# Optimization experiments

Measured on AMD Instinct MI355X. Metric: run time of the kernel, lower is better.

The kernel has to match this reference:

```python
import jax, jax.numpy as jnp
import numpy as np

B, T, D = 8, 512, 1024
H, DQK, DV = 16, 128, 128  # n_heads, d_qk = emb_dim//h_qk, d_v = emb_dim//h_v


def setup_inputs() -> dict:
    key = jax.random.key(0)
    ks = jax.random.split(key, 8)
    s = 0.02
    return {
        "X": jax.random.normal(ks[0], (B, T, D), jnp.float32),
        "pos_enc_k": jax.random.normal(ks[1], (T, T, DQK), jnp.float32) * s,
        "pos_enc_v": jax.random.normal(ks[2], (T, T, DV), jnp.float32) * s,
        "Wq": jax.random.normal(ks[3], (D, H * DQK), jnp.float32) * s,
        "bq": jnp.zeros((H * DQK,), jnp.float32),
        "Wk": jax.random.normal(ks[4], (D, H * DQK), jnp.float32) * s,
        "bk": jnp.zeros((H * DQK,), jnp.float32),
        "Wv": jax.random.normal(ks[5], (D, H * DV), jnp.float32) * s,
        "bv": jnp.zeros((H * DV,), jnp.float32),
        "Wp": jax.random.normal(ks[6], (H * DV, D), jnp.float32) * s,
        "bp": jnp.zeros((D,), jnp.float32),
    }


def reference(X, pos_enc_k, pos_enc_v, Wq, bq, Wk, bk, Wv, bv, Wp, bp):
    b, t, d = X.shape
    # projections -> (b, h, t, dhead)
    Q = (X @ Wq + bq).reshape(b, t, H, DQK).transpose(0, 2, 1, 3)
    K = (X @ Wk + bk).reshape(b, t, H, DQK).transpose(0, 2, 1, 3)
    V = (X @ Wv + bv).reshape(b, t, H, DV).transpose(0, 2, 1, 3)
    # content attention + relative-position key bias
    att = jnp.einsum("bhqd,bhkd->bhqk", Q, K)
    att = att + jnp.einsum("bhqd,qkd->bhqk", Q, pos_enc_k)
    att = att / jnp.sqrt(jnp.asarray(DQK, X.dtype))
    # causal mask (do_mask=True)
    causal = jnp.tril(jnp.ones((t, t), bool))
    att = jnp.where(causal[None, None], att, jnp.asarray(-jnp.inf, att.dtype))
    att = jax.nn.softmax(att, axis=-1)
    # values + relative-position value correction
    y = jnp.einsum("bhqk,bhkd->bhqd", att, V)
    y = y + jnp.einsum("bhqk,qkd->bhqd", att, pos_enc_v)
    y = y.transpose(0, 2, 1, 3).reshape(b, t, H * DV)
    return y @ Wp + bp
```

## Files before the change

### kernel.cpp

```cpp
#include <hip/hip_runtime.h>
#include <stdint.h>

#define B_  8
#define T_  512
#define D_  1024
#define H_  16
#define DH  128
#define BH  128
#define ND  2048
#define BT  4096

typedef __attribute__((ext_vector_type(8))) short          short8;
typedef __attribute__((ext_vector_type(8))) __bf16         bf16x8;
typedef __attribute__((ext_vector_type(4))) float          f32x4;
typedef __attribute__((ext_vector_type(4))) unsigned short ushort4v;

static __device__ __forceinline__ unsigned short f2bf(float f) {
  unsigned u = __builtin_bit_cast(unsigned, f);
  u += 0x7FFFu + ((u >> 16) & 1u);
  return (unsigned short)(u >> 16);
}
static __device__ __forceinline__ float bf2f(unsigned short h) {
  unsigned u = ((unsigned)h) << 16;
  return __builtin_bit_cast(float, u);
}
static __device__ __forceinline__ f32x4 mfma16(short8 a, short8 b, f32x4 c) {
  return __builtin_amdgcn_mfma_f32_16x16x32_bf16(
      __builtin_bit_cast(bf16x8, a), __builtin_bit_cast(bf16x8, b), c, 0, 0, 0);
}
static __device__ __forceinline__ void gload16(const unsigned short* g, unsigned short* l) {
  __builtin_amdgcn_global_load_lds(
      (const __attribute__((address_space(1))) void*)g,
      (__attribute__((address_space(3))) void*)l, 16, 0, 0);
}

template <int ROWS>
static __device__ __forceinline__ void stage_sw64(unsigned short* lds,
                                                  const unsigned short* __restrict__ src,
                                                  long stride, int tid) {
#pragma unroll
  for (int it = 0; it < ROWS / 32; ++it) {
    int n = tid + it * 256;
    int r = n >> 3, c = (n & 7) ^ (r & 7);
    gload16(src + (long)r * stride + c * 8, lds + n * 8);
  }
}

template <int MR, int NR>
static __device__ __forceinline__ void mfma_sw64(const unsigned short* As,
                                                 const unsigned short* Bs,
                                                 int a0, int b0, int lrow, int g,
                                                 f32x4 (*acc)[NR]) {
#pragma unroll
  for (int ks = 0; ks < 2; ++ks) {
    short8 a[MR], b[NR];
#pragma unroll
    for (int i = 0; i < MR; ++i) {
      int ra = a0 + i * 16 + lrow;
      int c = (ks * 4 + g) ^ (ra & 7);
      a[i] = *(const short8*)&As[ra * 64 + c * 8];
    }
#pragma unroll
    for (int j = 0; j < NR; ++j) {
      int rb = b0 + j * 16 + lrow;
      int c = (ks * 4 + g) ^ (rb & 7);
      b[j] = *(const short8*)&Bs[rb * 64 + c * 8];
    }
#pragma unroll
    for (int i = 0; i < MR; ++i)
#pragma unroll
      for (int j = 0; j < NR; ++j) acc[i][j] = mfma16(a[i], b[j], acc[i][j]);
  }
}

#define IDS4                             \
  const int tid  = threadIdx.x;          \
  const int lane = tid & 63;             \
  const int wid  = tid >> 6;             \
  const int lrow = lane & 15;            \
  const int lk8  = (lane >> 4) * 8;      \
  const int lr4  = (lane >> 4) * 4;      \
  const int lg   = lane >> 4;            \
  const int wm = wid >> 1, wn = wid & 1;

#define LTS 132
#define LTQ 68

__global__ __launch_bounds__(256) void k_prep(const float* __restrict__ X,
                                              unsigned short* __restrict__ Xb,
                                              const float* __restrict__ Wq,
                                              const float* __restrict__ Wk,
                                              const float* __restrict__ Wv,
                                              const float* __restrict__ Wp,
                                              unsigned short* __restrict__ WT,
                                              unsigned short* __restrict__ WpT) {
  __shared__ float tile[32][33];
  int bid = blockIdx.x;
  if (bid < 4096) {
    int i = bid * 256 + threadIdx.x;
    f32x4 v = ((const f32x4*)X)[i];
    ushort4v o;
    o.x = f2bf(v.x); o.y = f2bf(v.y); o.z = f2bf(v.z); o.w = f2bf(v.w);
    ((ushort4v*)Xb)[i] = o;
    return;
  }
  bid -= 4096;
  const int which = bid >> 11;
  const int local = bid & 2047;
  const float* in;
  unsigned short* outp;
  int R, C, bx, by;
  if (which < 3) {
    in = which == 0 ? Wq : (which == 1 ? Wk : Wv);
    outp = WT + (size_t)which * ND * D_;
    R = D_; C = ND; bx = local & 63; by = local >> 6;
  } else {
    in = Wp; outp = WpT;
    R = ND; C = D_; bx = local & 31; by = local >> 5;
  }
  int c0 = bx * 32, r0 = by * 32;
  int tx = threadIdx.x & 31, ty = threadIdx.x >> 5;
#pragma unroll
  for (int i = 0; i < 32; i += 8)
    tile[ty + i][tx] = in[(long)(r0 + ty + i) * C + (c0 + tx)];
  __syncthreads();
#pragma unroll
  for (int i = 0; i < 32; i += 8)
    outp[(long)(c0 + ty + i) * R + (r0 + tx)] = f2bf(tile[tx][ty + i]);
}

__global__ __launch_bounds__(256) void k_vtrans(const unsigned short* __restrict__ vin,
                                                unsigned short* __restrict__ vout) {
  __shared__ unsigned short tile[32][33];
  int bh = blockIdx.z;
  int t0 = blockIdx.x * 32, d0 = blockIdx.y * 32;
  int tx = threadIdx.x & 31, ty = threadIdx.x >> 5;
#pragma unroll
  for (int i = 0; i < 32; i += 8)
    tile[ty + i][tx] = vin[((long)bh * T_ + t0 + ty + i) * DH + (d0 + tx)];
  __syncthreads();
#pragma unroll
  for (int i = 0; i < 32; i += 8)
    vout[((long)bh * DH + (d0 + ty + i)) * T_ + (t0 + tx)] = tile[tx][ty + i];
}

__global__ __launch_bounds__(512, 1) void k_proj8(const unsigned short* __restrict__ Xb,
                                                  const unsigned short* __restrict__ WT,
                                                  const float* __restrict__ bq,
                                                  const float* __restrict__ bk,
                                                  const float* __restrict__ bv,
                                                  unsigned short* __restrict__ Qb,
                                                  unsigned short* __restrict__ Kb,
                                                  unsigned short* __restrict__ Vb) {
  __shared__ unsigned short lds[65536];
  const int tid  = threadIdx.x;
  const int lane = tid & 63;
  const int g    = lane >> 4;
  const int wid  = tid >> 6;
  const int wm   = wid >> 2;
  const int wn   = wid & 3;
  const int lrow = lane & 15;
  const int lr4  = g * 4;

  const int flat = blockIdx.x, xcd = flat & 7, local = flat >> 3;
  const int mt = local & 15;
  const int nt = xcd * 3 + (local >> 4);
  const int m0 = mt * 256, n0 = nt * 256;

  const unsigned short* Asrc = Xb + (long)m0 * D_;
  const unsigned short* Bsrc = WT + (long)n0 * D_;

  auto stage = [&](int t) {
    unsigned short* base = lds + (t & 1) * 32768;
    const unsigned short* as = Asrc + t * 64;
    const unsigned short* bs = Bsrc + t * 64;
#pragma unroll
    for (int it = 0; it < 4; ++it) {
      int n = tid + it * 512;
      int r = n >> 3, c = (n & 7) ^ (r & 7);
      gload16(as + (long)r * D_ + c * 8, base + n * 8);
    }
#pragma unroll
    for (int it = 0; it < 4; ++it) {
      int n = tid + it * 512;
      int r = n >> 3, c = (n & 7) ^ (r & 7);
      gload16(bs + (long)r * D_ + c * 8, base + 16384 + n * 8);
    }
  };

  stage(0);
  f32x4 acc[8][4] = {};
  for (int t = 0; t < 16; ++t) {
    const unsigned short* At = lds + (t & 1) * 32768;
    const unsigned short* Bt = At + 16384;
    if (t < 15) {
      stage(t + 1);
      asm volatile("s_waitcnt vmcnt(8)" ::: "memory");
    } else {
      asm volatile("s_waitcnt vmcnt(0)" ::: "memory");
    }
    __builtin_amdgcn_sched_barrier(0);
    __builtin_amdgcn_s_barrier();
#pragma unroll
    for (int p = 0; p < 4; ++p) {
      const int mh = p & 1, ks = p >> 1;
      short8 a[4], b[4];
#pragma unroll
      for (int i = 0; i < 4; ++i) {
        int ra = wm * 128 + mh * 64 + i * 16 + lrow;
        int c = (ks * 4 + g) ^ (ra & 7);
        a[i] = *(const short8*)&At[ra * 64 + c * 8];
      }
#pragma unroll
      for (int j = 0; j < 4; ++j) {
        int rb = wn * 64 + j * 16 + lrow;
        int c = (ks * 4 + g) ^ (rb & 7);
        b[j] = *(const short8*)&Bt[rb * 64 + c * 8];
      }
      asm volatile("s_waitcnt lgkmcnt(0)" ::: "memory");
      __builtin_amdgcn_sched_barrier(0);
      __builtin_amdgcn_s_setprio(1);
#pragma unroll
      for (int i = 0; i < 4; ++i)
#pragma unroll
        for (int j = 0; j < 4; ++j)
          acc[mh * 4 + i][j] = mfma16(a[i], b[j], acc[mh * 4 + i][j]);
      __builtin_amdgcn_s_setprio(0);
      __builtin_amdgcn_s_barrier();
    }
  }

  const int nb = n0 >> 11;
  const float* biasp = nb == 0 ? bq : (nb == 1 ? bk : bv);
  unsigned short* dst = nb == 0 ? Qb : (nb == 1 ? Kb : Vb);
#pragma unroll
  for (int i = 0; i < 8; ++i)
#pragma unroll
    for (int j = 0; j < 4; ++j) {
      int cc = (n0 & 2047) + wn * 64 + j * 16 + lrow;
      int h = cc >> 7, dd = cc & 127;
      float bias = biasp[cc];
#pragma unroll
      for (int r = 0; r < 4; ++r) {
        int m = m0 + wm * 128 + i * 16 + lr4 + r;
        int bb = m >> 9, tt = m & (T_ - 1);
        dst[((long)(bb * H_ + h) * T_ + tt) * DH + dd] = f2bf(acc[i][j][r] + bias);
      }
    }
}

__global__ __launch_bounds__(256) void k_posk(const unsigned short* __restrict__ Qb,
                                              const float* __restrict__ Pk,
                                              unsigned short* __restrict__ att) {
  const int bid = blockIdx.x;
  const int q = (bid & 1) ? (T_ - 1 - (bid >> 1)) : (bid >> 1);
  const int ktiles = (q >> 6) + 1;
  __shared__ unsigned short As[128 * 128];
  __shared__ unsigned short Bs[2][64 * 136];
  IDS4
  {
    const unsigned short* src = Qb + (long)q * DH;
#pragma unroll
    for (int it = 0; it < 8; ++it) {
      int n = tid + it * 256;
      int r = n >> 4, c = (n & 15) ^ (r & 7);
      gload16(src + (long)r * (T_ * DH) + c * 8, As + n * 8);
    }
  }
  f32x4 pv[8];
  const float* psrc = Pk + (long)q * T_ * DH;
  auto loadPk = [&](int kt) {
#pragma unroll
    for (int it = 0; it < 8; ++it) {
      int chunk = tid + it * 256;
      int r = chunk >> 5, c4 = (chunk & 31) * 4;
      pv[it] = *(const f32x4*)(psrc + (long)(kt * 64 + r) * DH + c4);
    }
  };
  auto writeB = [&](int buf) {
#pragma unroll
    for (int it = 0; it < 8; ++it) {
      int chunk = tid + it * 256;
      int r = chunk >> 5, c4 = (chunk & 31) * 4;
      ushort4v o;
      o.x = f2bf(pv[it].x); o.y = f2bf(pv[it].y); o.z = f2bf(pv[it].z); o.w = f2bf(pv[it].w);
      *(ushort4v*)&Bs[buf][r * 136 + c4] = o;
    }
  };
  loadPk(0);
  asm volatile("s_waitcnt vmcnt(0)" ::: "memory");
  writeB(0);
  asm volatile("s_waitcnt lgkmcnt(0)" ::: "memory");
  __builtin_amdgcn_s_barrier();
  for (int kt = 0; kt < ktiles; ++kt) {
    const bool pre = (kt + 1 < ktiles);
    if (pre) loadPk(kt + 1);
    f32x4 acc[4][2] = {};
#pragma unroll
    for (int ks = 0; ks < 4; ++ks) {
      short8 a[4], b[2];
#pragma unroll
      for (int i = 0; i < 4; ++i) {
        int ra = wm * 64 + i * 16 + lrow;
        int c = (ks * 4 + lg) ^ (ra & 7);
        a[i] = *(const short8*)&As[ra * 128 + c * 8];
      }
#pragma unroll
      for (int j = 0; j < 2; ++j)
        b[j] = *(const short8*)&Bs[kt & 1][(wn * 32 + j * 16 + lrow) * 136 + ks * 32 + lk8];
#pragma unroll
      for (int i = 0; i < 4; ++i)
#pragma unroll
        for (int j = 0; j < 2; ++j)
          acc[i][j] = mfma16(a[i], b[j], acc[i][j]);
    }
    if (pre) {
      asm volatile("s_waitcnt vmcnt(0)" ::: "memory");
      writeB((kt + 1) & 1);
    }
#pragma unroll
    for (int i = 0; i < 4; ++i)
#pragma unroll
      for (int j = 0; j < 2; ++j) {
        int k = kt * 64 + wn * 32 + j * 16 + lrow;
#pragma unroll
        for (int r = 0; r < 4; ++r) {
          int bh = wm * 64 + i * 16 + lr4 + r;
          att[((long)q * BH + bh) * T_ + k] = f2bf(acc[i][j][r]);
        }
      }
    asm volatile("s_waitcnt lgkmcnt(0)" ::: "memory");
    __builtin_amdgcn_s_barrier();
  }
}

__global__ __launch_bounds__(256) void k_qkv(const unsigned short* __restrict__ Qb,
                                             const unsigned short* __restrict__ Kb,
                                             const unsigned short* __restrict__ Vt,
                                             unsigned short* __restrict__ att,
                                             float* __restrict__ Sinv,
                                             unsigned short* __restrict__ Ybb) {
  const int bh = blockIdx.x & 127, pr = blockIdx.x >> 7;
  __shared__ unsigned short Qs[64 * 128], Ks[64 * 128], Vs[128 * 64];
  __shared__ unsigned short Ps[64 * 72];
  __shared__ float lt[64 * LTQ];
  __shared__ float sInv[64];
  const int tid = threadIdx.x;
  const int lane = tid & 63, wid = tid >> 6;
  const int wm = wid >> 1, wn = wid & 1;
  const int lrow = lane & 15, lk8 = (lane >> 4) * 8, lr4 = (lane >> 4) * 4;
  const int row = tid >> 2, c0 = (tid & 3) * 16;
  const float scale = 0.08838834764831845f;
  const int b = bh >> 4, h = bh & 15;

  for (int pass = 0; pass < 2; ++pass) {
    const int qt = pass ? 7 - pr : pr;
    const int q0 = qt * 64, ktiles = qt + 1;
    const int qabs = q0 + row;
    unsigned short* arow = att + ((long)qabs * BH + bh) * T_;
    {
      const unsigned short* src = Qb + ((long)bh * T_ + q0) * DH;
#pragma unroll
      for (int it = 0; it < 4; ++it) {
        int n = tid + it * 256;
        int r = n >> 4, c = (n & 15) ^ (r & 7);
        gload16(src + (long)r * DH + c * 8, Qs + n * 8);
      }
    }
    float ssum = 0.f;
    f32x4 accv[2][4] = {};
    for (int kt = 0; kt < ktiles; ++kt) {
      const unsigned short* ksrc = Kb + ((long)bh * T_ + kt * 64) * DH;
#pragma unroll
      for (int it = 0; it < 4; ++it) {
        int n = tid + it * 256;
        int r = n >> 4, c = (n & 15) ^ (r & 7);
        gload16(ksrc + (long)r * DH + c * 8, Ks + n * 8);
      }
      const unsigned short* vsrc = Vt + (long)bh * DH * T_ + kt * 64;
#pragma unroll
      for (int it = 0; it < 4; ++it) {
        int n = tid + it * 256;
        int r = n >> 3, c = (n & 7) ^ (r & 7);
        gload16(vsrc + (long)r * T_ + c * 8, Vs + n * 8);
      }
      short8 pb0 = *(const short8*)(arow + kt * 64 + c0);
      short8 pb1 = *(const short8*)(arow + kt * 64 + c0 + 8);
      __syncthreads();
      f32x4 acc[2][2] = {};
#pragma unroll
      for (int ks = 0; ks < 4; ++ks) {
        short8 aq[2], bk2[2];
#pragma unroll
        for (int i = 0; i < 2; ++i) {
          int ra = wm * 32 + i * 16 + lrow;
          int c = (ks * 4 + (lane >> 4)) ^ (ra & 7);
          aq[i] = *(const short8*)&Qs[ra * 128 + c * 8];
        }
#pragma unroll
        for (int j = 0; j < 2; ++j) {
          int rb = wn * 32 + j * 16 + lrow;
          int c = (ks * 4 + (lane >> 4)) ^ (rb & 7);
          bk2[j] = *(const short8*)&Ks[rb * 128 + c * 8];
        }
#pragma unroll
        for (int i = 0; i < 2; ++i)
#pragma unroll
          for (int j = 0; j < 2; ++j)
            acc[i][j] = mfma16(aq[i], bk2[j], acc[i][j]);
      }
#pragma unroll
      for (int i = 0; i < 2; ++i)
#pragma unroll
        for (int j = 0; j < 2; ++j)
#pragma unroll
          for (int r = 0; r < 4; ++r)
            lt[(wm * 32 + i * 16 + lr4 + r) * LTQ + wn * 32 + j * 16 + lrow] = acc[i][j][r];
      __syncthreads();
      short8 o0, o1;
#pragma unroll
      for (int jj = 0; jj < 8; ++jj) {
        int k = kt * 64 + c0 + jj;
        float e0 = (k <= qabs)
                   ? __expf((lt[row * LTQ + c0 + jj] + bf2f((unsigned short)pb0[jj])) * scale) : 0.f;
        float e1 = (k + 8 <= qabs)
                   ? __expf((lt[row * LTQ + c0 + 8 + jj] + bf2f((unsigned short)pb1[jj])) * scale) : 0.f;
        o0[jj] = (short)f2bf(e0);
        o1[jj] = (short)f2bf(e1);
        ssum += e0 + e1;
      }
      *(short8*)(arow + kt * 64 + c0) = o0;
      *(short8*)(arow + kt * 64 + c0 + 8) = o1;
      *(short8*)&Ps[row * 72 + c0] = o0;
      *(short8*)&Ps[row * 72 + c0 + 8] = o1;
      __syncthreads();
#pragma unroll
      for (int ks = 0; ks < 2; ++ks) {
        short8 ap[2], bv2[4];
#pragma unroll
        for (int i = 0; i < 2; ++i) {
          int ra = wm * 32 + i * 16 + lrow;
          ap[i] = *(const short8*)&Ps[ra * 72 + ks * 32 + lk8];
        }
#pragma unroll
        for (int j = 0; j < 4; ++j) {
          int rb = wn * 64 + j * 16 + lrow;
          int c = ((ks * 4) + (lane >> 4)) ^ (rb & 7);
          bv2[j] = *(const short8*)&Vs[rb * 64 + c * 8];
        }
#pragma unroll
        for (int i = 0; i < 2; ++i)
#pragma unroll
          for (int j = 0; j < 4; ++j)
            accv[i][j] = mfma16(ap[i], bv2[j], accv[i][j]);
      }
      __syncthreads();
    }
    ssum += __shfl_xor(ssum, 1, 64);
    ssum += __shfl_xor(ssum, 2, 64);
    float si = 1.f / ssum;
    if ((tid & 3) == 0) { sInv[row] = si; Sinv[(long)qabs * BH + bh] = si; }
    __syncthreads();
#pragma unroll
    for (int i = 0; i < 2; ++i) {
      float sc2[4];
#pragma unroll
      for (int r = 0; r < 4; ++r) sc2[r] = sInv[wm * 32 + i * 16 + lr4 + r];
#pragma unroll
      for (int j = 0; j < 4; ++j) {
        int d = wn * 64 + j * 16 + lrow;
#pragma unroll
        for (int r = 0; r < 4; ++r) {
          int q = q0 + wm * 32 + i * 16 + lr4 + r;
          Ybb[(long)(b * T_ + q) * ND + h * DH + d] = f2bf(accv[i][j][r] * sc2[r]);
        }
      }
    }
    __syncthreads();
  }
}

__global__ __launch_bounds__(256) void k_posv(const unsigned short* __restrict__ P,
                                              const float* __restrict__ Pv,
                                              const float* __restrict__ Sinv,
                                              unsigned short* __restrict__ Ybb) {
  const int bid = blockIdx.x;
  const int q = (bid & 1) ? (T_ - 1 - (bid >> 1)) : (bid >> 1);
  const int ktiles = (q >> 6) + 1;
  __shared__ unsigned short As[128 * 64];
  __shared__ unsigned short Bs[2][128 * 72];
  __shared__ float lt[64 * LTQ];
  IDS4
  f32x4 pv[8];
  const float* psrc = Pv + (long)q * T_ * DH;
  auto loadPv = [&](int kt) {
#pragma unroll
    for (int it = 0; it < 8; ++it) {
      int chunk = tid + it * 256;
      int d4 = (chunk & 3) * 4 + ((chunk >> 6) & 7) * 16;
      int k  = ((chunk >> 2) & 15) + ((chunk >> 9) & 3) * 16;
      pv[it] = *(const f32x4*)(psrc + (long)(kt * 64 + k) * DH + d4);
    }
  };
  auto writeB = [&](int buf) {
#pragma unroll
    for (int it = 0; it < 8; ++it) {
      int chunk = tid + it * 256;
      int d4 = (chunk & 3) * 4 + ((chunk >> 6) & 7) * 16;
      int k  = ((chunk >> 2) & 15) + ((chunk >> 9) & 3) * 16;
      Bs[buf][(d4 + 0) * 72 + k] = f2bf(pv[it].x);
      Bs[buf][(d4 + 1) * 72 + k] = f2bf(pv[it].y);
      Bs[buf][(d4 + 2) * 72 + k] = f2bf(pv[it].z);
      Bs[buf][(d4 + 3) * 72 + k] = f2bf(pv[it].w);
    }
  };
  loadPv(0);
  asm volatile("s_waitcnt vmcnt(0)" ::: "memory");
  writeB(0);
  asm volatile("s_waitcnt lgkmcnt(0)" ::: "memory");
  __builtin_amdgcn_s_barrier();
  f32x4 acc[4][4] = {};
  for (int kt = 0; kt < ktiles; ++kt) {
    const bool pre = (kt + 1 < ktiles);
    stage_sw64<128>(As, P + (long)q * BH * T_ + kt * 64, T_, tid);
    if (pre) loadPv(kt + 1);
    if (pre) asm volatile("s_waitcnt vmcnt(8)" ::: "memory");
    else     asm volatile("s_waitcnt vmcnt(0)" ::: "memory");
    __builtin_amdgcn_s_barrier();
#pragma unroll
    for (int ks = 0; ks < 2; ++ks) {
      short8 a[4], b[4];
#pragma unroll
      for (int i = 0; i < 4; ++i) {
        int ra = wm * 64 + i * 16 + lrow;
        int c = (ks * 4 + lg) ^ (ra & 7);
        a[i] = *(const short8*)&As[ra * 64 + c * 8];
      }
#pragma unroll
      for (int j = 0; j < 4; ++j)
        b[j] = *(const short8*)&Bs[kt & 1][(wn * 64 + j * 16 + lrow) * 72 + ks * 32 + lk8];
#pragma unroll
      for (int i = 0; i < 4; ++i)
#pragma unroll
        for (int j = 0; j < 4; ++j)
          acc[i][j] = mfma16(a[i], b[j], acc[i][j]);
    }
    if (pre) {
      asm volatile("s_waitcnt vmcnt(0)" ::: "memory");
      writeB((kt + 1) & 1);
    }
    asm volatile("s_waitcnt lgkmcnt(0)" ::: "memory");
    __builtin_amdgcn_s_barrier();
  }
  const int row = tid >> 2, c0 = (tid & 3) * 16;
#pragma unroll
  for (int hb = 0; hb < 2; ++hb)
#pragma unroll
    for (int hd = 0; hd < 2; ++hd) {
      int bh = hb * 64 + row;
      long idx = ((long)((bh >> 4) * T_ + q)) * ND + (bh & 15) * DH + hd * 64 + c0;
      short8 y0 = *(const short8*)&Ybb[idx];
      short8 y1 = *(const short8*)&Ybb[idx + 8];
      float sc = Sinv[(long)q * BH + bh];
      if (wm == hb && wn == hd) {
#pragma unroll
        for (int i = 0; i < 4; ++i)
#pragma unroll
          for (int j = 0; j < 4; ++j)
#pragma unroll
            for (int r = 0; r < 4; ++r)
              lt[(i * 16 + lr4 + r) * LTQ + j * 16 + lrow] = acc[i][j][r];
      }
      __syncthreads();
      short8 o0, o1;
#pragma unroll
      for (int jj = 0; jj < 8; ++jj) {
        o0[jj] = (short)f2bf(lt[row * LTQ + c0 + jj] * sc + bf2f((unsigned short)y0[jj]));
        o1[jj] = (short)f2bf(lt[row * LTQ + c0 + 8 + jj] * sc + bf2f((unsigned short)y1[jj]));
      }
      *(short8*)&Ybb[idx] = o0;
      *(short8*)&Ybb[idx + 8] = o1;
      __syncthreads();
    }
}

__global__ __launch_bounds__(256) void k_oproj(const unsigned short* __restrict__ Ybb,
                                               const unsigned short* __restrict__ WpT,
                                               const float* __restrict__ bp,
                                               float* __restrict__ outp) {
  __shared__ unsigned short As[128 * 64], Bs[128 * 64];
  IDS4
  const int m0 = blockIdx.y * 128, n0 = blockIdx.x * 128;
  f32x4 acc[4][4] = {};
  for (int kk = 0; kk < ND; kk += 64) {
    stage_sw64<128>(As, Ybb + (long)m0 * ND + kk, ND, tid);
    stage_sw64<128>(Bs, WpT + (long)n0 * ND + kk, ND, tid);
    __syncthreads();
    mfma_sw64<4, 4>(As, Bs, wm * 64, wn * 64, lrow, lg, acc);
    __syncthreads();
  }
  float* lt = (float*)As;
  const int row = tid >> 4, c8 = (tid & 15) * 8;
  f32x4 b0 = *(const f32x4*)(bp + n0 + c8);
  f32x4 b1 = *(const f32x4*)(bp + n0 + c8 + 4);
#pragma unroll
  for (int rr = 0; rr < 8; ++rr) {
    if (wm == (rr >> 2)) {
      const int ii = rr & 3;
#pragma unroll
      for (int j = 0; j < 4; ++j)
#pragma unroll
        for (int r = 0; r < 4; ++r)
          lt[(lr4 + r) * LTS + wn * 64 + j * 16 + lrow] = acc[ii][j][r];
    }
    __syncthreads();
    f32x4 v0 = *(const f32x4*)&lt[row * LTS + c8];
    f32x4 v1 = *(const f32x4*)&lt[row * LTS + c8 + 4];
    int m = m0 + rr * 16 + row;
    v0.x += b0.x; v0.y += b0.y; v0.z += b0.z; v0.w += b0.w;
    v1.x += b1.x; v1.y += b1.y; v1.z += b1.z; v1.w += b1.w;
    *(f32x4*)&outp[(long)m * D_ + n0 + c8] = v0;
    *(f32x4*)&outp[(long)m * D_ + n0 + c8 + 4] = v1;
    __syncthreads();
  }
}

extern "C" void kernel_launch(void* const* d_in, const int* in_sizes, int n_in,
                              void* d_out, int out_size, void* d_ws, size_t ws_size,
                              hipStream_t stream) {
  const float* X  = (const float*)d_in[0];
  const float* Pk = (const float*)d_in[1];
  const float* Pv = (const float*)d_in[2];
  const float* Wq = (const float*)d_in[3];
  const float* bq = (const float*)d_in[4];
  const float* Wk = (const float*)d_in[5];
  const float* bk = (const float*)d_in[6];
  const float* Wv = (const float*)d_in[7];
  const float* bv = (const float*)d_in[8];
  const float* Wp = (const float*)d_in[9];
  const float* bp = (const float*)d_in[10];
  float* out = (float*)d_out;

  uint8_t* w = (uint8_t*)d_ws;
  unsigned short* Xb  = (unsigned short*)w; w += (size_t)BT * D_ * 2;
  unsigned short* WT  = (unsigned short*)w; w += (size_t)3 * ND * D_ * 2;
  unsigned short* WpT = (unsigned short*)w; w += (size_t)D_ * ND * 2;
  unsigned short* Qb  = (unsigned short*)w; w += (size_t)BH * T_ * DH * 2;
  unsigned short* Kb  = (unsigned short*)w; w += (size_t)BH * T_ * DH * 2;
  unsigned short* Vb  = (unsigned short*)w; w += (size_t)BH * T_ * DH * 2;
  unsigned short* Vt  = (unsigned short*)w; w += (size_t)BH * DH * T_ * 2;
  unsigned short* att = (unsigned short*)w; w += (size_t)T_ * BH * T_ * 2;
  unsigned short* Ybb = (unsigned short*)w; w += (size_t)BT * ND * 2;
  float*          Sinv= (float*)w;          w += (size_t)T_ * BH * 4;

  k_prep<<<12288, 256, 0, stream>>>(X, Xb, Wq, Wk, Wv, Wp, WT, WpT);
  k_proj8<<<384, 512, 0, stream>>>(Xb, WT, bq, bk, bv, Qb, Kb, Vb);
  k_vtrans<<<dim3(T_ / 32, DH / 32, BH), 256, 0, stream>>>(Vb, Vt);
  k_posk<<<T_, 256, 0, stream>>>(Qb, Pk, att);
  k_qkv<<<512, 256, 0, stream>>>(Qb, Kb, Vt, att, Sinv, Ybb);
  k_posv<<<T_, 256, 0, stream>>>(att, Pv, Sinv, Ybb);
  k_oproj<<<dim3(D_ / 128, BT / 128), 256, 0, stream>>>(Ybb, WpT, bp, out);
}
```

Before: 248.3 us.

## Replace pipelined 256x256 projection GEMM with simple 128x128 single-buffered tiles

The QKV projection kernel drops its 512-thread, 256x256-tile, double-buffered, swizzled-LDS pipeline. In its place is a 256-thread kernel with 128x128 tiles, a single LDS buffer, plain unswizzled row-major LDS layout, and __syncthreads around each k-step. Four times as many blocks are launched, which adds parallelism and occupancy. In exchange it loses load/compute overlap and per-tile data reuse, and it may suffer LDS bank conflicts.

```diff
diff --git a/kernel.cpp b/kernel.cpp
--- a/kernel.cpp
+++ b/kernel.cpp
@@ -34,6 +34,19 @@
       (__attribute__((address_space(3))) void*)l, 16, 0, 0);
 }
 
+template <int ROWS, int COLS>
+static __device__ __forceinline__ void stage_gl2(unsigned short* lds,
+                                                 const unsigned short* __restrict__ src,
+                                                 long stride, int tid) {
+  constexpr int CPR = COLS / 8;
+#pragma unroll
+  for (int it = 0; it < ROWS * COLS / 8 / 256; ++it) {
+    int chunk = tid + it * 256;
+    int r = chunk / CPR, c8 = (chunk % CPR) * 8;
+    gload16(src + (long)r * stride + c8, lds + chunk * 8);
+  }
+}
+
 template <int ROWS>
 static __device__ __forceinline__ void stage_sw64(unsigned short* lds,
                                                   const unsigned short* __restrict__ src,
@@ -43,6 +56,25 @@
     int n = tid + it * 256;
     int r = n >> 3, c = (n & 7) ^ (r & 7);
     gload16(src + (long)r * stride + c * 8, lds + n * 8);
+  }
+}
+
+template <int MR, int NR, int LDA, int LDB, int KD>
+static __device__ __forceinline__ void mfma_blk(const unsigned short* As,
+                                                const unsigned short* Bs,
+                                                int a0, int b0, int lrow, int lk8,
+                                                f32x4 (*acc)[NR]) {
+#pragma unroll
+  for (int ks = 0; ks < KD; ks += 32) {
+    short8 a[MR], b[NR];
+#pragma unroll
+    for (int i = 0; i < MR; ++i) a[i] = *(const short8*)&As[(a0 + i * 16 + lrow) * LDA + ks + lk8];
+#pragma unroll
+    for (int j = 0; j < NR; ++j) b[j] = *(const short8*)&Bs[(b0 + j * 16 + lrow) * LDB + ks + lk8];
+#pragma unroll
+    for (int i = 0; i < MR; ++i)
+#pragma unroll
+      for (int j = 0; j < NR; ++j) acc[i][j] = mfma16(a[i], b[j], acc[i][j]);
   }
 }
 
@@ -144,107 +176,46 @@
     vout[((long)bh * DH + (d0 + ty + i)) * T_ + (t0 + tx)] = tile[tx][ty + i];
 }
 
-__global__ __launch_bounds__(512, 1) void k_proj8(const unsigned short* __restrict__ Xb,
-                                                  const unsigned short* __restrict__ WT,
-                                                  const float* __restrict__ bq,
-                                                  const float* __restrict__ bk,
-                                                  const float* __restrict__ bv,
-                                                  unsigned short* __restrict__ Qb,
-                                                  unsigned short* __restrict__ Kb,
-                                                  unsigned short* __restrict__ Vb) {
-  __shared__ unsigned short lds[65536];
-  const int tid  = threadIdx.x;
-  const int lane = tid & 63;
-  const int g    = lane >> 4;
-  const int wid  = tid >> 6;
-  const int wm   = wid >> 2;
-  const int wn   = wid & 3;
-  const int lrow = lane & 15;
-  const int lr4  = g * 4;
-
+__global__ __launch_bounds__(256) void k_proj8(const unsigned short* __restrict__ Xb,
+                                               const unsigned short* __restrict__ WT,
+                                               const float* __restrict__ bq,
+                                               const float* __restrict__ bk,
+                                               const float* __restrict__ bv,
+                                               unsigned short* __restrict__ Qb,
+                                               unsigned short* __restrict__ Kb,
+                                               unsigned short* __restrict__ Vb) {
+  __shared__ unsigned short As[128 * 64], Bs[128 * 64];
+  IDS4
   const int flat = blockIdx.x, xcd = flat & 7, local = flat >> 3;
-  const int mt = local & 15;
-  const int nt = xcd * 3 + (local >> 4);
-  const int m0 = mt * 256, n0 = nt * 256;
-
-  const unsigned short* Asrc = Xb + (long)m0 * D_;
-  const unsigned short* Bsrc = WT + (long)n0 * D_;
-
-  auto stage = [&](int t) {
-    unsigned short* base = lds + (t & 1) * 32768;
-    const unsigned short* as = Asrc + t * 64;
-    const unsigned short* bs = Bsrc + t * 64;
-#pragma unroll
-    for (int it = 0; it < 4; ++it) {
-      int n = tid + it * 512;
-      int r = n >> 3, c = (n & 7) ^ (r & 7);
-      gload16(as + (long)r * D_ + c * 8, base + n * 8);
-    }
-#pragma unroll
-    for (int it = 0; it < 4; ++it) {
-      int n = tid + it * 512;
-      int r = n >> 3, c = (n & 7) ^ (r & 7);
-      gload16(bs + (long)r * D_ + c * 8, base + 16384 + n * 8);
-    }
-  };
-
-  stage(0);
-  f32x4 acc[8][4] = {};
-  for (int t = 0; t < 16; ++t) {
-    const unsigned short* At = lds + (t & 1) * 32768;
-    const unsigned short* Bt = At + 16384;
-    if (t < 15) {
-      stage(t + 1);
-      asm volatile("s_waitcnt vmcnt(8)" ::: "memory");
-    } else {
-      asm volatile("s_waitcnt vmcnt(0)" ::: "memory");
-    }
-    __builtin_amdgcn_sched_barrier(0);
-    __builtin_amdgcn_s_barrier();
-#pragma unroll
-    for (int p = 0; p < 4; ++p) {
-      const int mh = p & 1, ks = p >> 1;
-      short8 a[4], b[4];
-#pragma unroll
-      for (int i = 0; i < 4; ++i) {
-        int ra = wm * 128 + mh * 64 + i * 16 + lrow;
-        int c = (ks * 4 + g) ^ (ra & 7);
-        a[i] = *(const short8*)&At[ra * 64 + c * 8];
-      }
-#pragma unroll
-      for (int j = 0; j < 4; ++j) {
-        int rb = wn * 64 + j * 16 + lrow;
-        int c = (ks * 4 + g) ^ (rb & 7);
-        b[j] = *(const short8*)&Bt[rb * 64 + c * 8];
-      }
-      asm volatile("s_waitcnt lgkmcnt(0)" ::: "memory");
-      __builtin_amdgcn_sched_barrier(0);
-      __builtin_amdgcn_s_setprio(1);
-#pragma unroll
-      for (int i = 0; i < 4; ++i)
-#pragma unroll
-        for (int j = 0; j < 4; ++j)
-          acc[mh * 4 + i][j] = mfma16(a[i], b[j], acc[mh * 4 + i][j]);
-      __builtin_amdgcn_s_setprio(0);
-      __builtin_amdgcn_s_barrier();
-    }
+  const int nt = xcd * 6 + (local % 6);
+  const int mt = local / 6;
+  const int m0 = mt * 128, n0 = nt * 128;
+
+  f32x4 acc[4][4] = {};
+  for (int kk = 0; kk < D_; kk += 64) {
+    stage_gl2<128, 64>(As, Xb + (long)m0 * D_ + kk, D_, tid);
+    stage_gl2<128, 64>(Bs, WT + (long)n0 * D_ + kk, D_, tid);
+    __syncthreads();
+    mfma_blk<4, 4, 64, 64, 64>(As, Bs, wm * 64, wn * 64, lrow, lk8, acc);
+    __syncthreads();
   }
 
   const int nb = n0 >> 11;
   const float* biasp = nb == 0 ? bq : (nb == 1 ? bk : bv);
   unsigned short* dst = nb == 0 ? Qb : (nb == 1 ? Kb : Vb);
-#pragma unroll
-  for (int i = 0; i < 8; ++i)
+  const int hcol = (n0 & 2047) >> 7;
+#pragma unroll
+  for (int i = 0; i < 4; ++i)
 #pragma unroll
     for (int j = 0; j < 4; ++j) {
       int cc = (n0 & 2047) + wn * 64 + j * 16 + lrow;
-      int h = cc >> 7, dd = cc & 127;
+      int dd = cc & 127;
       float bias = biasp[cc];
 #pragma unroll
       for (int r = 0; r < 4; ++r) {
-        int m = m0 + wm * 128 + i * 16 + lr4 + r;
+        int m = m0 + wm * 64 + i * 16 + lr4 + r;
         int bb = m >> 9, tt = m & (T_ - 1);
-        dst[((long)(bb * H_ + h) * T_ + tt) * DH + dd] = f2bf(acc[i][j][r] + bias);
+        dst[((long)(bb * H_ + hcol) * T_ + tt) * DH + dd] = f2bf(acc[i][j][r] + bias);
       }
     }
 }
@@ -654,7 +625,7 @@
   float*          Sinv= (float*)w;          w += (size_t)T_ * BH * 4;
 
   k_prep<<<12288, 256, 0, stream>>>(X, Xb, Wq, Wk, Wv, Wp, WT, WpT);
-  k_proj8<<<384, 512, 0, stream>>>(Xb, WT, bq, bk, bv, Qb, Kb, Vb);
+  k_proj8<<<1536, 256, 0, stream>>>(Xb, WT, bq, bk, bv, Qb, Kb, Vb);
   k_vtrans<<<dim3(T_ / 32, DH / 32, BH), 256, 0, stream>>>(Vb, Vt);
   k_posk<<<T_, 256, 0, stream>>>(Qb, Pk, att);
   k_qkv<<<512, 256, 0, stream>>>(Qb, Kb, Vt, att, Sinv, Ybb);
```

Result: slower. 255.6 us (+2.9%).
